# Performance work log

Hardware: AMD Instinct MI355X
Metric: run time of the kernel (lower is better)

## Reference

```python
import jax, jax.numpy as jnp
from jax import lax
import numpy as np

D_STATE = 16
DT_RANK = 16
D_INNER = 512
D_MODEL = 256


def _silu(x):
    return x * jax.nn.sigmoid(x)


def _ln(x, g, b):
    mu = jnp.mean(x, -1, keepdims=True)
    v = jnp.mean((x - mu) ** 2, -1, keepdims=True)
    return (x - mu) / jnp.sqrt(v + 1e-5) * g + b


def _mamba(x, Win, Wc, bc, Wx, Wdt, bdt, Alog, Dp, Wout):
    # x: [B, T, 256]; mamba_ssm defaults: expand=2, d_state=16, d_conv=4
    B, T, _ = x.shape
    xz = x @ Win.T                       # [B,T,1024]
    xc, z = jnp.split(xz, 2, axis=-1)    # each [B,T,512]
    # causal depthwise conv over time
    xt = jnp.transpose(xc, (0, 2, 1))    # [B,512,T]
    xt = lax.conv_general_dilated(xt, Wc[:, None, :], (1,), [(3, 0)],
                                  feature_group_count=D_INNER,
                                  dimension_numbers=('NCH', 'OIH', 'NCH'))
    xc = _silu(jnp.transpose(xt + bc[None, :, None], (0, 2, 1)))  # [B,T,512]
    dbl = xc @ Wx.T                      # [B,T,48]
    dt = jax.nn.softplus(dbl[..., :DT_RANK] @ Wdt.T + bdt)        # [B,T,512]
    Bm = dbl[..., DT_RANK:DT_RANK + D_STATE]                      # [B,T,16]
    Cm = dbl[..., DT_RANK + D_STATE:]                             # [B,T,16]
    A = -jnp.exp(Alog)                   # [512,16]
    dA = jnp.exp(dt[..., None] * A)                               # [B,T,512,16]
    dBu = dt[..., None] * Bm[:, :, None, :] * xc[..., None]       # [B,T,512,16]

    def step(h, inp):
        dA_t, dBu_t, C_t = inp
        h = dA_t * h + dBu_t
        return h, jnp.einsum('bdn,bn->bd', h, C_t)

    h0 = jnp.zeros((B, D_INNER, D_STATE), x.dtype)
    _, ys = lax.scan(step, h0, (jnp.moveaxis(dA, 1, 0),
                                jnp.moveaxis(dBu, 1, 0),
                                jnp.moveaxis(Cm, 1, 0)))
    y = jnp.moveaxis(ys, 0, 1) + xc * Dp
    y = y * _silu(z)
    return y @ Wout.T


def _forward(x1, x2, x3, x4, audio_feature,
             ln_g, ln_b, in_proj_w, conv_w, conv_b, xproj_w,
             dt_w, dt_b, A_log, D, out_proj_w, gate_w, gate_b):
    bt = x1.shape[0]
    gates = []
    for i in range(4):          # 4 independent 3-layer Mamba encoders
        a = audio_feature
        for l in range(3):      # Mamba_channel_temporal_block: a = ln(a); a = a + mamba(a)
            a = _ln(a, ln_g[i, l], ln_b[i, l])
            a = a + _mamba(a, in_proj_w[i, l], conv_w[i, l], conv_b[i, l],
                           xproj_w[i, l], dt_w[i, l], dt_b[i, l],
                           A_log[i, l], D[i, l], out_proj_w[i, l])
        gates.append(_silu(a @ gate_w[i].T + gate_b[i]))  # [B,5,256]
    g1 = gates[0].reshape(bt, 256, 1, 1)
    g2 = jnp.transpose(gates[1], (1, 0, 2)).reshape(bt, 256, 1, 1)
    g3 = jnp.transpose(gates[2], (1, 0, 2)).reshape(bt, 256, 1, 1)
    g4 = jnp.transpose(gates[3], (1, 0, 2)).reshape(bt, 256, 1, 1)
    o1 = x1 + g1 * x1   # gamma = 1
    o2 = x2 + g2 * x2
    o3 = x3 + g3 * x3
    o4 = x4 + g4 * x4
    audio_flat = audio_feature.reshape(-1, D_MODEL)[:, :, None]  # [bt,256,1]
    return (o4, o3, o2, o1, audio_flat)


def setup_inputs() -> dict:
    key = jax.random.key(0)
    ks = jax.random.split(key, 16)
    f32 = jnp.float32
    inp = {
        'x1': jax.random.normal(ks[0], (80, 256, 56, 56), f32),
        'x2': jax.random.normal(ks[1], (80, 256, 28, 28), f32),
        'x3': jax.random.normal(ks[2], (80, 256, 14, 14), f32),
        'x4': jax.random.normal(ks[3], (80, 256, 7, 7), f32),
        'audio_feature': jax.random.normal(ks[4], (16, 5, 256), f32),
        'ln_g': jnp.ones((4, 3, 256), f32),
        'ln_b': jnp.zeros((4, 3, 256), f32),
        'in_proj_w': jax.random.normal(ks[5], (4, 3, 2 * D_INNER, 256), f32) * 0.02,
        'conv_w': jax.random.normal(ks[6], (4, 3, D_INNER, 4), f32) * 0.1,
        'conv_b': jax.random.normal(ks[7], (4, 3, D_INNER), f32) * 0.02,
        'xproj_w': jax.random.normal(ks[8], (4, 3, DT_RANK + 2 * D_STATE, D_INNER), f32) * 0.02,
        'dt_w': jax.random.normal(ks[9], (4, 3, D_INNER, DT_RANK), f32) * 0.02,
        'dt_b': jax.random.normal(ks[10], (4, 3, D_INNER), f32) * 0.1 - 2.0,
        'A_log': jnp.log(jnp.tile(jnp.arange(1, D_STATE + 1, dtype=f32), (4, 3, D_INNER, 1))),
        'D': jnp.ones((4, 3, D_INNER), f32),
        'out_proj_w': jax.random.normal(ks[11], (4, 3, 256, D_INNER), f32) * 0.02,
        'gate_w': jax.random.normal(ks[12], (4, 256, 256), f32) * 0.05,
        'gate_b': jnp.zeros((4, 256), f32),
    }
    return inp


def reference(x1, x2, x3, x4, audio_feature,
              ln_g, ln_b, in_proj_w, conv_w, conv_b, xproj_w,
              dt_w, dt_b, A_log, D, out_proj_w, gate_w, gate_b):
    return _forward(x1, x2, x3, x4, audio_feature,
                    ln_g, ln_b, in_proj_w, conv_w, conv_b, xproj_w,
                    dt_w, dt_b, A_log, D, out_proj_w, gate_w, gate_b)
```

## Files before the change

### kernel.cpp

```cpp
#include <hip/hip_runtime.h>
#include <hip/hip_bf16.h>
#include <math.h>


#define NTOK 80
#define DM   256
#define DI   512

typedef float f32x4 __attribute__((ext_vector_type(4)));

__device__ __forceinline__ float silu_f(float v) {
    return v / (1.f + expf(-v));
}
__device__ __forceinline__ float dot4v(f32x4 a, f32x4 b) {
    return a.x*b.x + a.y*b.y + a.z*b.z + a.w*b.w;
}
__device__ __forceinline__ unsigned pack2bf(float lo, float hi) {
    unsigned ul = __float_as_uint(lo), uh = __float_as_uint(hi);
    unsigned bl = (ul + 0x7FFFu + ((ul >> 16) & 1u)) >> 16;
    unsigned bh = (uh + 0x7FFFu + ((uh >> 16) & 1u)) >> 16;
    return bl | (bh << 16);
}
__device__ __forceinline__ f32x4 unpk4(unsigned x, unsigned y) {
    f32x4 r;
    r.x = __uint_as_float(x << 16); r.y = __uint_as_float(x & 0xFFFF0000u);
    r.z = __uint_as_float(y << 16); r.w = __uint_as_float(y & 0xFFFF0000u);
    return r;
}

#define OFF_SG    0
#define OFF_WIN8  81920
#define OFF_WOUT8 1654784
#define OFF_GW8   2441216
#define OFF_WXT   2572288
#define OFF_DBLP  2867200
#define OFF_OUTP  2928640
#define OFF_BAR   3256320

__global__ __launch_bounds__(256) void k_tr(const float* __restrict__ Win,
                                            const float* __restrict__ Wout,
                                            const float* __restrict__ Wx,
                                            const float* __restrict__ gw,
                                            float* __restrict__ ws) {
    __shared__ __align__(16) float SH[8256];
    int b = blockIdx.x, tid = threadIdx.x;
    if (b == 0) {
        unsigned* barp = (unsigned*)(ws + OFF_BAR);
        #pragma unroll
        for (int j = 0; j < 4; ++j) barp[j * 256 + tid] = 0u;
    }

    if (b < 608) {
        const float* src; unsigned* dst; int rowStride, Ctot, c0, k0;
        if (b < 384) {
            int il = b / 32, rest = b % 32, cb = rest >> 1, kh = rest & 1;
            src = Win + (size_t)il * 1024 * 256; rowStride = 256; Ctot = 1024;
            c0 = cb * 64; k0 = kh * 128;
            dst = (unsigned*)(ws + OFF_WIN8) + (size_t)il * 32768 * 4;
        } else if (b < 576) {
            int t = b - 384; int il = t / 16, rest = t % 16, cb = rest >> 2, kq = rest & 3;
            src = Wout + (size_t)il * 256 * 512; rowStride = 512; Ctot = 256;
            c0 = cb * 64; k0 = kq * 128;
            dst = (unsigned*)(ws + OFF_WOUT8) + (size_t)il * 16384 * 4;
        } else {
            int t = b - 576; int i = t / 8, rest = t % 8, cb = rest >> 1, kh = rest & 1;
            src = gw + (size_t)i * 256 * 256; rowStride = 256; Ctot = 256;
            c0 = cb * 64; k0 = kh * 128;
            dst = (unsigned*)(ws + OFF_GW8) + (size_t)i * 8192 * 4;
        }
        for (int idx = tid; idx < 64 * 32; idx += 256) {
            int row = idx >> 5, kq4 = idx & 31;
            const float4 v = *(const float4*)(src + (size_t)(c0 + row) * rowStride
                                              + k0 + kq4 * 4);
            float* f = SH + row * 129 + kq4 * 4;
            f[0] = v.x; f[1] = v.y; f[2] = v.z; f[3] = v.w;
        }
        __syncthreads();
        uint4* d4 = (uint4*)dst;
        for (int idx = tid; idx < 1024; idx += 256) {
            int k8l = idx >> 6, c = idx & 63;
            const float* f = SH + c * 129 + k8l * 8;
            uint4 o;
            o.x = pack2bf(f[0], f[1]); o.y = pack2bf(f[2], f[3]);
            o.z = pack2bf(f[4], f[5]); o.w = pack2bf(f[6], f[7]);
            d4[((size_t)(k0 / 8 + k8l)) * Ctot + c0 + c] = o;
        }
    } else {
        int bb = b - 608; int mat = bb >> 3, tile = bb & 7;
        const float4* src = (const float4*)Wx + (size_t)mat * 6144;
        float4* dst = (float4*)(ws + OFF_WXT) + (size_t)mat * 6144;
        int R = 48, C4 = 128, tilesC = 4;
        int r0 = (tile / tilesC) << 5, cc0 = (tile % tilesC) << 5;
        float4* t4 = (float4*)SH;
        int tx = tid & 31, ty = tid >> 5;
        #pragma unroll
        for (int j = 0; j < 4; ++j) {
            int r = ty + j * 8;
            if (r0 + r < R) t4[r * 33 + tx] = src[(size_t)(r0 + r) * C4 + cc0 + tx];
        }
        __syncthreads();
        #pragma unroll
        for (int j = 0; j < 4; ++j) {
            int cc = ty + j * 8;
            if (r0 + tx < R) dst[(size_t)(cc0 + cc) * R + r0 + tx] = t4[tx * 33 + cc];
        }
    }
}

__device__ __forceinline__ void gbar(unsigned* slot) {
    __syncthreads();
    if (threadIdx.x == 0) {
        __hip_atomic_fetch_add(slot, 1u, __ATOMIC_RELEASE, __HIP_MEMORY_SCOPE_AGENT);
        while (__hip_atomic_load(slot, __ATOMIC_RELAXED, __HIP_MEMORY_SCOPE_AGENT) < 4u)
            __builtin_amdgcn_s_sleep(1);
        (void)__hip_atomic_load(slot, __ATOMIC_ACQUIRE, __HIP_MEMORY_SCOPE_AGENT);
    }
    __syncthreads();
}

__global__ __launch_bounds__(512) void k_chain4b(
    const float* __restrict__ audio,
    const float* __restrict__ ln_g, const float* __restrict__ ln_b,
    const float* __restrict__ Wc,   const float* __restrict__ bc,
    const float* __restrict__ Wdt,  const float* __restrict__ bdt,
    const float* __restrict__ Alog, const float* __restrict__ Dp,
    const float* __restrict__ gb,   float* __restrict__ ws)
{
    int gid = blockIdx.x & 63;
    int q   = blockIdx.x >> 6;
    int i = gid & 3, b = gid >> 2;
    int tid = threadIdx.x, lane = tid & 63, wave = tid >> 6;
    int dq = q * 128;

    float* s_g  = ws + OFF_SG;
    float* dblp = ws + OFF_DBLP + (size_t)gid * 4 * 240;
    float* outp = ws + OFF_OUTP + (size_t)gid * 4 * 1280;
    unsigned* bar = (unsigned*)(ws + OFF_BAR) + gid * 16;

    __shared__ __align__(16) float a_l   [1280];
    __shared__ __align__(16) float aln_l [1280];
    __shared__ __align__(16) float xz_l  [1280];
    __shared__ __align__(16) float xc_l  [640];
    __shared__ __align__(16) float y_l   [640];
    __shared__ __align__(16) float dbl_l [240];
    __shared__ __align__(16) float xp_l  [480];
    __shared__ __align__(16) float part_l[5120];

    if (tid < 320)
        ((f32x4*)a_l)[tid] = ((const f32x4*)(audio + (size_t)b * 1280))[tid];
    __syncthreads();

    for (int l = 0; l < 3; ++l) {
        int il = i * 3 + l;

        if (wave < 5) {
            f32x4 x = ((f32x4*)a_l)[wave*64 + lane];
            float s = x.x + x.y + x.z + x.w;
            #pragma unroll
            for (int o = 32; o > 0; o >>= 1) s += __shfl_down(s, o, 64);
            float mu = __shfl(s, 0, 64) * (1.f/256.f);
            f32x4 d = x - mu;
            float v2 = d.x*d.x + d.y*d.y + d.z*d.z + d.w*d.w;
            #pragma unroll
            for (int o = 32; o > 0; o >>= 1) v2 += __shfl_down(v2, o, 64);
            float rstd = rsqrtf(__shfl(v2, 0, 64) * (1.f/256.f) + 1e-5f);
            f32x4 g4 = ((const f32x4*)(ln_g + (size_t)il*DM))[lane];
            f32x4 b4 = ((const f32x4*)(ln_b + (size_t)il*DM))[lane];
            ((f32x4*)aln_l)[wave*64 + lane] = d * rstd * g4 + b4;
        }
        __syncthreads();

        {
            int cp = tid & 127, kq = tid >> 7;
            int lc, cA;
            if (cp < 64) { lc = 2*cp;       cA = dq + 2*cp; }
            else         { lc = 2*cp;       cA = 512 + dq + 2*(cp-64); }
            const uint4* W8 = (const uint4*)(ws + OFF_WIN8) + (size_t)il * 32768;
            const f32x4* a4 = (const f32x4*)aln_l;
            float accA[5] = {0,0,0,0,0}, accB[5] = {0,0,0,0,0};
            #pragma unroll
            for (int j = 0; j < 8; ++j) {
                int k8 = kq*8 + j;
                uint4 wa = W8[(size_t)k8*1024 + cA];
                uint4 wb = W8[(size_t)k8*1024 + cA + 1];
                f32x4 wa0 = unpk4(wa.x, wa.y), wa1 = unpk4(wa.z, wa.w);
                f32x4 wb0 = unpk4(wb.x, wb.y), wb1 = unpk4(wb.z, wb.w);
                #pragma unroll
                for (int r = 0; r < 5; ++r) {
                    f32x4 a0 = a4[r*64 + k8*2], a1 = a4[r*64 + k8*2 + 1];
                    accA[r] += dot4v(wa0, a0) + dot4v(wa1, a1);
                    accB[r] += dot4v(wb0, a0) + dot4v(wb1, a1);
                }
            }
            #pragma unroll
            for (int r = 0; r < 5; ++r) {
                part_l[kq*1280 + r*256 + lc]     = accA[r];
                part_l[kq*1280 + r*256 + lc + 1] = accB[r];
            }
        }
        __syncthreads();
        for (int v = tid; v < 1280; v += 512)
            xz_l[v] = part_l[v] + part_l[1280+v] + part_l[2560+v] + part_l[3840+v];
        __syncthreads();

        for (int v = tid; v < 640; v += 512) {
            int r = v >> 7, dl = v & 127;
            int ch = dq + dl;
            const float* wr = Wc + ((size_t)il*DI + ch)*4;
            float acc = bc[(size_t)il*DI + ch] + wr[3]*xz_l[r*256 + dl];
            if (r >= 1) acc += wr[2]*xz_l[(r-1)*256 + dl];
            if (r >= 2) acc += wr[1]*xz_l[(r-2)*256 + dl];
            if (r >= 3) acc += wr[0]*xz_l[(r-3)*256 + dl];
            xc_l[r*128 + dl] = silu_f(acc);
        }
        __syncthreads();

        if (tid < 480) {
            int c = tid % 48, r = (tid / 48) % 5, kh = tid / 240;
            const f32x4* wp = (const f32x4*)(ws + OFF_WXT) + (size_t)il*6144 + c;
            const f32x4* x4 = (const f32x4*)xc_l + r*32 + kh*16;
            float acc = 0.f;
            #pragma unroll
            for (int kk = 0; kk < 16; ++kk)
                acc += dot4v(wp[(size_t)(q*32 + kh*16 + kk)*48], x4[kk]);
            xp_l[tid] = acc;
        }
        __syncthreads();
        if (tid < 240) dblp[q*240 + tid] = xp_l[tid] + xp_l[240 + tid];
        gbar(bar + 2*l);
        if (tid < 240)
            dbl_l[tid] = dblp[tid] + dblp[240+tid] + dblp[480+tid] + dblp[720+tid];
        __syncthreads();

        if (tid < 128) {
            int d = dq + tid;
            float A[16], h[16];
            const f32x4* al4 = (const f32x4*)(Alog + ((size_t)il*DI + d)*16);
            f32x4 av0 = al4[0], av1 = al4[1], av2 = al4[2], av3 = al4[3];
            A[0]=-expf(av0.x); A[1]=-expf(av0.y); A[2]=-expf(av0.z); A[3]=-expf(av0.w);
            A[4]=-expf(av1.x); A[5]=-expf(av1.y); A[6]=-expf(av1.z); A[7]=-expf(av1.w);
            A[8]=-expf(av2.x); A[9]=-expf(av2.y); A[10]=-expf(av2.z); A[11]=-expf(av2.w);
            A[12]=-expf(av3.x); A[13]=-expf(av3.y); A[14]=-expf(av3.z); A[15]=-expf(av3.w);
            #pragma unroll
            for (int n = 0; n < 16; ++n) h[n] = 0.f;
            const f32x4* wd4 = (const f32x4*)(Wdt + ((size_t)il*DI + d)*16);
            f32x4 w0 = wd4[0], w1 = wd4[1], w2 = wd4[2], w3 = wd4[3];
            float bdtv = bdt[(size_t)il*DI + d];
            float dv   = Dp[(size_t)il*DI + d];
            #pragma unroll
            for (int t = 0; t < 5; ++t) {
                const float* db = dbl_l + t*48;
                float acc = bdtv;
                acc += db[0]*w0.x + db[1]*w0.y + db[2]*w0.z + db[3]*w0.w;
                acc += db[4]*w1.x + db[5]*w1.y + db[6]*w1.z + db[7]*w1.w;
                acc += db[8]*w2.x + db[9]*w2.y + db[10]*w2.z + db[11]*w2.w;
                acc += db[12]*w3.x + db[13]*w3.y + db[14]*w3.z + db[15]*w3.w;
                float dtv = fmaxf(acc, 0.f) + log1pf(expf(-fabsf(acc)));
                float xv  = xc_l[t*128 + tid];
                float zv  = xz_l[t*256 + 128 + tid];
                float dx  = dtv * xv;
                float yacc = 0.f;
                #pragma unroll
                for (int n = 0; n < 16; ++n) {
                    h[n] = expf(dtv*A[n])*h[n] + dx*db[16 + n];
                    yacc += h[n]*db[32 + n];
                }
                y_l[t*128 + tid] = (yacc + xv*dv) * silu_f(zv);
            }
        }
        __syncthreads();

        {
            int cp = tid & 127, kq = tid >> 7;
            int cA = 2*cp;
            const uint4* W8 = (const uint4*)(ws + OFF_WOUT8) + (size_t)il * 16384;
            const f32x4* y4 = (const f32x4*)y_l;
            float accA[5] = {0,0,0,0,0}, accB[5] = {0,0,0,0,0};
            #pragma unroll
            for (int j = 0; j < 4; ++j) {
                int k8l = kq*4 + j;
                int k8g = q*16 + k8l;
                uint4 wa = W8[(size_t)k8g*256 + cA];
                uint4 wb = W8[(size_t)k8g*256 + cA + 1];
                f32x4 wa0 = unpk4(wa.x, wa.y), wa1 = unpk4(wa.z, wa.w);
                f32x4 wb0 = unpk4(wb.x, wb.y), wb1 = unpk4(wb.z, wb.w);
                #pragma unroll
                for (int r = 0; r < 5; ++r) {
                    f32x4 y0 = y4[r*32 + k8l*2], y1 = y4[r*32 + k8l*2 + 1];
                    accA[r] += dot4v(wa0, y0) + dot4v(wa1, y1);
                    accB[r] += dot4v(wb0, y0) + dot4v(wb1, y1);
                }
            }
            #pragma unroll
            for (int r = 0; r < 5; ++r) {
                part_l[kq*1280 + r*256 + cA]     = accA[r];
                part_l[kq*1280 + r*256 + cA + 1] = accB[r];
            }
        }
        __syncthreads();
        for (int v = tid; v < 1280; v += 512)
            outp[q*1280 + v] = part_l[v] + part_l[1280+v] + part_l[2560+v] + part_l[3840+v];
        gbar(bar + 2*l + 1);
        for (int v = tid; v < 1280; v += 512)
            a_l[v] = aln_l[v] + outp[v] + outp[1280+v] + outp[2560+v] + outp[3840+v];
        __syncthreads();
    }

    {
        int cp = tid & 31, kq = tid >> 5;
        int gA = q*64 + 2*cp;
        const uint4* G8 = (const uint4*)(ws + OFF_GW8) + (size_t)i * 8192;
        const f32x4* a4 = (const f32x4*)a_l;
        float accA[5] = {0,0,0,0,0}, accB[5] = {0,0,0,0,0};
        #pragma unroll
        for (int j = 0; j < 2; ++j) {
            int k8 = kq*2 + j;
            uint4 wa = G8[(size_t)k8*256 + gA];
            uint4 wb = G8[(size_t)k8*256 + gA + 1];
            f32x4 wa0 = unpk4(wa.x, wa.y), wa1 = unpk4(wa.z, wa.w);
            f32x4 wb0 = unpk4(wb.x, wb.y), wb1 = unpk4(wb.z, wb.w);
            #pragma unroll
            for (int r = 0; r < 5; ++r) {
                f32x4 a0 = a4[r*64 + k8*2], a1 = a4[r*64 + k8*2 + 1];
                accA[r] += dot4v(wa0, a0) + dot4v(wa1, a1);
                accB[r] += dot4v(wb0, a0) + dot4v(wb1, a1);
            }
        }
        #pragma unroll
        for (int r = 0; r < 5; ++r) {
            part_l[kq*320 + r*64 + 2*cp]     = accA[r];
            part_l[kq*320 + r*64 + 2*cp + 1] = accB[r];
        }
    }
    __syncthreads();
    if (tid < 320) {
        int r = tid >> 6, lc = tid & 63;
        float s = gb[(size_t)i*DM + q*64 + lc];
        #pragma unroll
        for (int kq = 0; kq < 16; ++kq) s += part_l[kq*320 + tid];
        int row = b*5 + r;
        int np  = (i == 0) ? row : (r*16 + b);
        s_g[((size_t)i*NTOK + np)*DM + q*64 + lc] = 1.f + silu_f(s);
    }
}

__global__ __launch_bounds__(256) void k_elem(
    const float* __restrict__ x1, const float* __restrict__ x2,
    const float* __restrict__ x3, const float* __restrict__ x4,
    const float* __restrict__ audio, const float* __restrict__ s_g,
    float* __restrict__ out) {
    int b = blockIdx.x;
    int t = threadIdx.x;

    if (b < 512) {
        const float* s = s_g + 3 * NTOK * DM;
        const f32x4* xv = (const f32x4*)x4;
        f32x4* ov = (f32x4*)out;
        const int total4 = 1003520 / 4;
        for (int v = b * 256 + t; v < total4; v += 512 * 256) {
            f32x4 x = __builtin_nontemporal_load(&xv[v]);
#pragma unroll
            for (int j = 0; j < 4; ++j) {
                int idx = v * 4 + j;
                x[j] *= s[idx / 49];
            }
            __builtin_nontemporal_store(x, &ov[v]);
        }
    } else if (b < 1024) {
        const float* s = s_g + 2 * NTOK * DM;
        const f32x4* xv = (const f32x4*)x3;
        f32x4* ov = (f32x4*)(out + 1003520);
        const int total4 = 4014080 / 4;
        for (int v = (b - 512) * 256 + t; v < total4; v += 512 * 256) {
            float f = s[v / 49];
            f32x4 x = __builtin_nontemporal_load(&xv[v]);
            x *= f;
            __builtin_nontemporal_store(x, &ov[v]);
        }
    } else if (b < 2048) {
        const float* s = s_g + 1 * NTOK * DM;
        const f32x4* xv = (const f32x4*)x2;
        f32x4* ov = (f32x4*)(out + 5017600);
        const int total4 = 16056320 / 4;
        for (int v = (b - 1024) * 256 + t; v < total4; v += 1024 * 256) {
            float f = s[v / 196];
            f32x4 x = __builtin_nontemporal_load(&xv[v]);
            x *= f;
            __builtin_nontemporal_store(x, &ov[v]);
        }
    } else if (b < 6144) {
        const float* s = s_g;
        const f32x4* xv = (const f32x4*)x1;
        f32x4* ov = (f32x4*)(out + 21073920);
        const int total4 = 64225280 / 4;
        for (int v = (b - 2048) * 256 + t; v < total4; v += 4096 * 256) {
            float f = s[v / 784];
            f32x4 x = __builtin_nontemporal_load(&xv[v]);
            x *= f;
            __builtin_nontemporal_store(x, &ov[v]);
        }
    } else {
        int idx = (b - 6144) * 256 + t;
        out[85299200 + idx] = audio[idx];
    }
}

extern "C" void kernel_launch(void* const* d_in, const int* in_sizes, int n_in,
                              void* d_out, int out_size, void* d_ws, size_t ws_size,
                              hipStream_t stream) {
    const float* x1        = (const float*)d_in[0];
    const float* x2        = (const float*)d_in[1];
    const float* x3        = (const float*)d_in[2];
    const float* x4        = (const float*)d_in[3];
    const float* audio     = (const float*)d_in[4];
    const float* ln_g      = (const float*)d_in[5];
    const float* ln_b      = (const float*)d_in[6];
    const float* in_proj_w = (const float*)d_in[7];
    const float* conv_w    = (const float*)d_in[8];
    const float* conv_b    = (const float*)d_in[9];
    const float* xproj_w   = (const float*)d_in[10];
    const float* dt_w      = (const float*)d_in[11];
    const float* dt_b      = (const float*)d_in[12];
    const float* A_log     = (const float*)d_in[13];
    const float* Dvec      = (const float*)d_in[14];
    const float* out_proj_w= (const float*)d_in[15];
    const float* gate_w    = (const float*)d_in[16];
    const float* gate_b    = (const float*)d_in[17];

    float* ws = (float*)d_ws;

    k_tr<<<704, 256, 0, stream>>>(in_proj_w, out_proj_w, xproj_w, gate_w, ws);
    k_chain4b<<<256, 512, 0, stream>>>(audio, ln_g, ln_b, conv_w, conv_b,
                                       dt_w, dt_b, A_log, Dvec, gate_b, ws);
    k_elem<<<6224, 256, 0, stream>>>(x1, x2, x3, x4, audio, ws + OFF_SG,
                                     (float*)d_out);
}
```

Baseline: 238.9 us.

## Merge four cooperating blocks per chain into one 1024-thread block, drop global barriers

Each (batch, encoder) chain previously ran on four 512-thread blocks that exchanged partial results through global memory with atomic spin barriers twice per layer. Now one 1024-thread block handles the full 512-channel width, so the barriers, global partial buffers and barrier reset go away. The GEMV inner loops are also restructured to 4 columns per lane with a cross-lane shuffle reduction instead of shared-memory partial sums. The cost is only 64 blocks on the GPU, so less parallelism for the weight streaming and the selective scan. Each thread also carries more serial work.

After: 554.0 us. +131.9%, slower.

```diff
diff --git a/kernel.cpp b/kernel.cpp
--- a/kernel.cpp
+++ b/kernel.cpp
@@ -33,9 +33,6 @@
 #define OFF_WOUT8 1654784
 #define OFF_GW8   2441216
 #define OFF_WXT   2572288
-#define OFF_DBLP  2867200
-#define OFF_OUTP  2928640
-#define OFF_BAR   3256320
 
 __global__ __launch_bounds__(256) void k_tr(const float* __restrict__ Win,
                                             const float* __restrict__ Wout,
@@ -44,11 +41,6 @@
                                             float* __restrict__ ws) {
     __shared__ __align__(16) float SH[8256];
     int b = blockIdx.x, tid = threadIdx.x;
-    if (b == 0) {
-        unsigned* barp = (unsigned*)(ws + OFF_BAR);
-        #pragma unroll
-        for (int j = 0; j < 4; ++j) barp[j * 256 + tid] = 0u;
-    }
 
     if (b < 608) {
         const float* src; unsigned* dst; int rowStride, Ctot, c0, k0;
@@ -107,18 +99,7 @@
     }
 }
 
-__device__ __forceinline__ void gbar(unsigned* slot) {
-    __syncthreads();
-    if (threadIdx.x == 0) {
-        __hip_atomic_fetch_add(slot, 1u, __ATOMIC_RELEASE, __HIP_MEMORY_SCOPE_AGENT);
-        while (__hip_atomic_load(slot, __ATOMIC_RELAXED, __HIP_MEMORY_SCOPE_AGENT) < 4u)
-            __builtin_amdgcn_s_sleep(1);
-        (void)__hip_atomic_load(slot, __ATOMIC_ACQUIRE, __HIP_MEMORY_SCOPE_AGENT);
-    }
-    __syncthreads();
-}
-
-__global__ __launch_bounds__(512) void k_chain4b(
+__global__ __launch_bounds__(1024, 4) void k_chain1k(
     const float* __restrict__ audio,
     const float* __restrict__ ln_g, const float* __restrict__ ln_b,
     const float* __restrict__ Wc,   const float* __restrict__ bc,
@@ -126,25 +107,19 @@
     const float* __restrict__ Alog, const float* __restrict__ Dp,
     const float* __restrict__ gb,   float* __restrict__ ws)
 {
-    int gid = blockIdx.x & 63;
-    int q   = blockIdx.x >> 6;
-    int i = gid & 3, b = gid >> 2;
-    int tid = threadIdx.x, lane = tid & 63, wave = tid >> 6;
-    int dq = q * 128;
-
-    float* s_g  = ws + OFF_SG;
-    float* dblp = ws + OFF_DBLP + (size_t)gid * 4 * 240;
-    float* outp = ws + OFF_OUTP + (size_t)gid * 4 * 1280;
-    unsigned* bar = (unsigned*)(ws + OFF_BAR) + gid * 16;
-
-    __shared__ __align__(16) float a_l   [1280];
-    __shared__ __align__(16) float aln_l [1280];
-    __shared__ __align__(16) float xz_l  [1280];
-    __shared__ __align__(16) float xc_l  [640];
-    __shared__ __align__(16) float y_l   [640];
-    __shared__ __align__(16) float dbl_l [240];
-    __shared__ __align__(16) float xp_l  [480];
-    __shared__ __align__(16) float part_l[5120];
+    int blk = blockIdx.x;
+    int i = blk & 3, b = blk >> 2;
+    int tid = threadIdx.x, lane = tid & 63, wv = tid >> 6;
+
+    float* s_g = ws + OFF_SG;
+
+    __shared__ __align__(16) float a_l  [1280];
+    __shared__ __align__(16) float aln_l[1280];
+    __shared__ __align__(16) float xz_l [5120];
+    __shared__ __align__(16) float xc_l [2560];
+    __shared__ __align__(16) float y_l  [2560];
+    __shared__ __align__(16) float dbl_l[240];
+    __shared__ __align__(16) float xp_l [960];
 
     if (tid < 320)
         ((f32x4*)a_l)[tid] = ((const f32x4*)(audio + (size_t)b * 1280))[tid];
@@ -153,8 +128,8 @@
     for (int l = 0; l < 3; ++l) {
         int il = i * 3 + l;
 
-        if (wave < 5) {
-            f32x4 x = ((f32x4*)a_l)[wave*64 + lane];
+        if (wv < 5) {
+            f32x4 x = ((f32x4*)a_l)[wv*64 + lane];
             float s = x.x + x.y + x.z + x.w;
             #pragma unroll
             for (int o = 32; o > 0; o >>= 1) s += __shfl_down(s, o, 64);
@@ -166,74 +141,84 @@
             float rstd = rsqrtf(__shfl(v2, 0, 64) * (1.f/256.f) + 1e-5f);
             f32x4 g4 = ((const f32x4*)(ln_g + (size_t)il*DM))[lane];
             f32x4 b4 = ((const f32x4*)(ln_b + (size_t)il*DM))[lane];
-            ((f32x4*)aln_l)[wave*64 + lane] = d * rstd * g4 + b4;
+            ((f32x4*)aln_l)[wv*64 + lane] = d * rstd * g4 + b4;
         }
         __syncthreads();
 
         {
-            int cp = tid & 127, kq = tid >> 7;
-            int lc, cA;
-            if (cp < 64) { lc = 2*cp;       cA = dq + 2*cp; }
-            else         { lc = 2*cp;       cA = 512 + dq + 2*(cp-64); }
+            int cq = lane & 15, kq = lane >> 4;
+            int col0 = wv * 64 + cq * 4;
             const uint4* W8 = (const uint4*)(ws + OFF_WIN8) + (size_t)il * 32768;
             const f32x4* a4 = (const f32x4*)aln_l;
-            float accA[5] = {0,0,0,0,0}, accB[5] = {0,0,0,0,0};
-            #pragma unroll
-            for (int j = 0; j < 8; ++j) {
-                int k8 = kq*8 + j;
-                uint4 wa = W8[(size_t)k8*1024 + cA];
-                uint4 wb = W8[(size_t)k8*1024 + cA + 1];
-                f32x4 wa0 = unpk4(wa.x, wa.y), wa1 = unpk4(wa.z, wa.w);
-                f32x4 wb0 = unpk4(wb.x, wb.y), wb1 = unpk4(wb.z, wb.w);
+            float acc[5][4];
+            #pragma unroll
+            for (int r = 0; r < 5; ++r)
+                #pragma unroll
+                for (int j = 0; j < 4; ++j) acc[r][j] = 0.f;
+            #pragma unroll
+            for (int t8 = 0; t8 < 8; ++t8) {
+                int k8 = kq * 8 + t8;
+                f32x4 wl[4], wh[4];
+                #pragma unroll
+                for (int j = 0; j < 4; ++j) {
+                    uint4 w = W8[(size_t)k8 * 1024 + col0 + j];
+                    wl[j] = unpk4(w.x, w.y); wh[j] = unpk4(w.z, w.w);
+                }
                 #pragma unroll
                 for (int r = 0; r < 5; ++r) {
-                    f32x4 a0 = a4[r*64 + k8*2], a1 = a4[r*64 + k8*2 + 1];
-                    accA[r] += dot4v(wa0, a0) + dot4v(wa1, a1);
-                    accB[r] += dot4v(wb0, a0) + dot4v(wb1, a1);
-                }
-            }
-            #pragma unroll
-            for (int r = 0; r < 5; ++r) {
-                part_l[kq*1280 + r*256 + lc]     = accA[r];
-                part_l[kq*1280 + r*256 + lc + 1] = accB[r];
-            }
-        }
-        __syncthreads();
-        for (int v = tid; v < 1280; v += 512)
-            xz_l[v] = part_l[v] + part_l[1280+v] + part_l[2560+v] + part_l[3840+v];
-        __syncthreads();
-
-        for (int v = tid; v < 640; v += 512) {
-            int r = v >> 7, dl = v & 127;
-            int ch = dq + dl;
-            const float* wr = Wc + ((size_t)il*DI + ch)*4;
-            float acc = bc[(size_t)il*DI + ch] + wr[3]*xz_l[r*256 + dl];
-            if (r >= 1) acc += wr[2]*xz_l[(r-1)*256 + dl];
-            if (r >= 2) acc += wr[1]*xz_l[(r-2)*256 + dl];
-            if (r >= 3) acc += wr[0]*xz_l[(r-3)*256 + dl];
-            xc_l[r*128 + dl] = silu_f(acc);
-        }
-        __syncthreads();
-
-        if (tid < 480) {
+                    f32x4 x0 = a4[r*64 + k8*2], x1 = a4[r*64 + k8*2 + 1];
+                    #pragma unroll
+                    for (int j = 0; j < 4; ++j)
+                        acc[r][j] += dot4v(wl[j], x0) + dot4v(wh[j], x1);
+                }
+            }
+            #pragma unroll
+            for (int r = 0; r < 5; ++r)
+                #pragma unroll
+                for (int j = 0; j < 4; ++j) {
+                    float v = acc[r][j];
+                    v += __shfl_xor(v, 16, 64);
+                    v += __shfl_xor(v, 32, 64);
+                    acc[r][j] = v;
+                }
+            if (kq == 0) {
+                #pragma unroll
+                for (int r = 0; r < 5; ++r) {
+                    f32x4 o = {acc[r][0], acc[r][1], acc[r][2], acc[r][3]};
+                    ((f32x4*)xz_l)[r*256 + (col0 >> 2)] = o;
+                }
+            }
+        }
+        __syncthreads();
+
+        for (int v = tid; v < 2560; v += 1024) {
+            int r = v >> 9, dl = v & 511;
+            const float* wr = Wc + ((size_t)il*DI + dl)*4;
+            float acc = bc[(size_t)il*DI + dl] + wr[3]*xz_l[r*1024 + dl];
+            if (r >= 1) acc += wr[2]*xz_l[(r-1)*1024 + dl];
+            if (r >= 2) acc += wr[1]*xz_l[(r-2)*1024 + dl];
+            if (r >= 3) acc += wr[0]*xz_l[(r-3)*1024 + dl];
+            xc_l[r*512 + dl] = silu_f(acc);
+        }
+        __syncthreads();
+
+        if (tid < 960) {
             int c = tid % 48, r = (tid / 48) % 5, kh = tid / 240;
             const f32x4* wp = (const f32x4*)(ws + OFF_WXT) + (size_t)il*6144 + c;
-            const f32x4* x4 = (const f32x4*)xc_l + r*32 + kh*16;
+            const f32x4* x4 = (const f32x4*)xc_l + r*128 + kh*32;
             float acc = 0.f;
             #pragma unroll
-            for (int kk = 0; kk < 16; ++kk)
-                acc += dot4v(wp[(size_t)(q*32 + kh*16 + kk)*48], x4[kk]);
+            for (int kk = 0; kk < 32; ++kk)
+                acc += dot4v(wp[(size_t)(kh*32 + kk)*48], x4[kk]);
             xp_l[tid] = acc;
         }
         __syncthreads();
-        if (tid < 240) dblp[q*240 + tid] = xp_l[tid] + xp_l[240 + tid];
-        gbar(bar + 2*l);
         if (tid < 240)
-            dbl_l[tid] = dblp[tid] + dblp[240+tid] + dblp[480+tid] + dblp[720+tid];
-        __syncthreads();
-
-        if (tid < 128) {
-            int d = dq + tid;
+            dbl_l[tid] = xp_l[tid] + xp_l[240+tid] + xp_l[480+tid] + xp_l[720+tid];
+        __syncthreads();
+
+        if (tid < 512) {
+            int d = tid;
             float A[16], h[16];
             const f32x4* al4 = (const f32x4*)(Alog + ((size_t)il*DI + d)*16);
             f32x4 av0 = al4[0], av1 = al4[1], av2 = al4[2], av3 = al4[3];
@@ -256,8 +241,8 @@
                 acc += db[8]*w2.x + db[9]*w2.y + db[10]*w2.z + db[11]*w2.w;
                 acc += db[12]*w3.x + db[13]*w3.y + db[14]*w3.z + db[15]*w3.w;
                 float dtv = fmaxf(acc, 0.f) + log1pf(expf(-fabsf(acc)));
-                float xv  = xc_l[t*128 + tid];
-                float zv  = xz_l[t*256 + 128 + tid];
+                float xv  = xc_l[t*512 + d];
+                float zv  = xz_l[t*1024 + 512 + d];
                 float dx  = dtv * xv;
                 float yacc = 0.f;
                 #pragma unroll
@@ -265,82 +250,119 @@
                     h[n] = expf(dtv*A[n])*h[n] + dx*db[16 + n];
                     yacc += h[n]*db[32 + n];
                 }
-                y_l[t*128 + tid] = (yacc + xv*dv) * silu_f(zv);
+                y_l[t*512 + d] = (yacc + xv*dv) * silu_f(zv);
             }
         }
         __syncthreads();
 
         {
-            int cp = tid & 127, kq = tid >> 7;
-            int cA = 2*cp;
+            int cq = lane & 15, kqi = lane >> 4;
+            int qg = (wv & 3) * 16 + cq;
+            int kg = wv >> 2;
+            int kq = kg * 4 + kqi;
+            int col0 = qg * 4;
             const uint4* W8 = (const uint4*)(ws + OFF_WOUT8) + (size_t)il * 16384;
             const f32x4* y4 = (const f32x4*)y_l;
-            float accA[5] = {0,0,0,0,0}, accB[5] = {0,0,0,0,0};
-            #pragma unroll
-            for (int j = 0; j < 4; ++j) {
-                int k8l = kq*4 + j;
-                int k8g = q*16 + k8l;
-                uint4 wa = W8[(size_t)k8g*256 + cA];
-                uint4 wb = W8[(size_t)k8g*256 + cA + 1];
-                f32x4 wa0 = unpk4(wa.x, wa.y), wa1 = unpk4(wa.z, wa.w);
-                f32x4 wb0 = unpk4(wb.x, wb.y), wb1 = unpk4(wb.z, wb.w);
+            float acc[5][4];
+            #pragma unroll
+            for (int r = 0; r < 5; ++r)
+                #pragma unroll
+                for (int j = 0; j < 4; ++j) acc[r][j] = 0.f;
+            #pragma unroll
+            for (int t8 = 0; t8 < 4; ++t8) {
+                int k8 = kq * 4 + t8;
+                f32x4 wl[4], wh[4];
+                #pragma unroll
+                for (int j = 0; j < 4; ++j) {
+                    uint4 w = W8[(size_t)k8 * 256 + col0 + j];
+                    wl[j] = unpk4(w.x, w.y); wh[j] = unpk4(w.z, w.w);
+                }
                 #pragma unroll
                 for (int r = 0; r < 5; ++r) {
-                    f32x4 y0 = y4[r*32 + k8l*2], y1 = y4[r*32 + k8l*2 + 1];
-                    accA[r] += dot4v(wa0, y0) + dot4v(wa1, y1);
-                    accB[r] += dot4v(wb0, y0) + dot4v(wb1, y1);
-                }
-            }
-            #pragma unroll
-            for (int r = 0; r < 5; ++r) {
-                part_l[kq*1280 + r*256 + cA]     = accA[r];
-                part_l[kq*1280 + r*256 + cA + 1] = accB[r];
-            }
-        }
-        __syncthreads();
-        for (int v = tid; v < 1280; v += 512)
-            outp[q*1280 + v] = part_l[v] + part_l[1280+v] + part_l[2560+v] + part_l[3840+v];
-        gbar(bar + 2*l + 1);
-        for (int v = tid; v < 1280; v += 512)
-            a_l[v] = aln_l[v] + outp[v] + outp[1280+v] + outp[2560+v] + outp[3840+v];
+                    f32x4 x0 = y4[r*128 + k8*2], x1 = y4[r*128 + k8*2 + 1];
+                    #pragma unroll
+                    for (int j = 0; j < 4; ++j)
+                        acc[r][j] += dot4v(wl[j], x0) + dot4v(wh[j], x1);
+                }
+            }
+            #pragma unroll
+            for (int r = 0; r < 5; ++r)
+                #pragma unroll
+                for (int j = 0; j < 4; ++j) {
+                    float v = acc[r][j];
+                    v += __shfl_xor(v, 16, 64);
+                    v += __shfl_xor(v, 32, 64);
+                    acc[r][j] = v;
+                }
+            if (kqi == 0) {
+                #pragma unroll
+                for (int r = 0; r < 5; ++r) {
+                    f32x4 o = {acc[r][0], acc[r][1], acc[r][2], acc[r][3]};
+                    ((f32x4*)xz_l)[kg*320 + r*64 + qg] = o;
+                }
+            }
+        }
+        __syncthreads();
+        for (int v = tid; v < 1280; v += 1024)
+            a_l[v] = aln_l[v] + xz_l[v] + xz_l[1280+v] + xz_l[2560+v] + xz_l[3840+v];
         __syncthreads();
     }
 
     {
-        int cp = tid & 31, kq = tid >> 5;
-        int gA = q*64 + 2*cp;
+        int cq = lane & 15, kqi = lane >> 4;
+        int qg = (wv & 3) * 16 + cq;
+        int kg = wv >> 2;
+        int kq = kg * 4 + kqi;
+        int col0 = qg * 4;
         const uint4* G8 = (const uint4*)(ws + OFF_GW8) + (size_t)i * 8192;
         const f32x4* a4 = (const f32x4*)a_l;
-        float accA[5] = {0,0,0,0,0}, accB[5] = {0,0,0,0,0};
+        float acc[5][4];
         #pragma unroll
-        for (int j = 0; j < 2; ++j) {
-            int k8 = kq*2 + j;
-            uint4 wa = G8[(size_t)k8*256 + gA];
-            uint4 wb = G8[(size_t)k8*256 + gA + 1];
-            f32x4 wa0 = unpk4(wa.x, wa.y), wa1 = unpk4(wa.z, wa.w);
-            f32x4 wb0 = unpk4(wb.x, wb.y), wb1 = unpk4(wb.z, wb.w);
+        for (int r = 0; r < 5; ++r)
+            #pragma unroll
+            for (int j = 0; j < 4; ++j) acc[r][j] = 0.f;
+        #pragma unroll
+        for (int t8 = 0; t8 < 2; ++t8) {
+            int k8 = kq * 2 + t8;
+            f32x4 wl[4], wh[4];
+            #pragma unroll
+            for (int j = 0; j < 4; ++j) {
+                uint4 w = G8[(size_t)k8 * 256 + col0 + j];
+                wl[j] = unpk4(w.x, w.y); wh[j] = unpk4(w.z, w.w);
+            }
             #pragma unroll
             for (int r = 0; r < 5; ++r) {
-                f32x4 a0 = a4[r*64 + k8*2], a1 = a4[r*64 + k8*2 + 1];
-                accA[r] += dot4v(wa0, a0) + dot4v(wa1, a1);
-                accB[r] += dot4v(wb0, a0) + dot4v(wb1, a1);
+                f32x4 x0 = a4[r*64 + k8*2], x1 = a4[r*64 + k8*2 + 1];
+                #pragma unroll
+                for (int j = 0; j < 4; ++j)
+                    acc[r][j] += dot4v(wl[j], x0) + dot4v(wh[j], x1);
             }
         }
         #pragma unroll
-        for (int r = 0; r < 5; ++r) {
-            part_l[kq*320 + r*64 + 2*cp]     = accA[r];
-            part_l[kq*320 + r*64 + 2*cp + 1] = accB[r];
+        for (int r = 0; r < 5; ++r)
+            #pragma unroll
+            for (int j = 0; j < 4; ++j) {
+                float v = acc[r][j];
+                v += __shfl_xor(v, 16, 64);
+                v += __shfl_xor(v, 32, 64);
+                acc[r][j] = v;
+            }
+        if (kqi == 0) {
+            #pragma unroll
+            for (int r = 0; r < 5; ++r) {
+                f32x4 o = {acc[r][0], acc[r][1], acc[r][2], acc[r][3]};
+                ((f32x4*)xz_l)[kg*320 + r*64 + qg] = o;
+            }
         }
     }
     __syncthreads();
-    if (tid < 320) {
-        int r = tid >> 6, lc = tid & 63;
-        float s = gb[(size_t)i*DM + q*64 + lc];
-        #pragma unroll
-        for (int kq = 0; kq < 16; ++kq) s += part_l[kq*320 + tid];
+    for (int v = tid; v < 1280; v += 1024) {
+        int r = v >> 8, c = v & 255;
+        float val = gb[(size_t)i*DM + c]
+                  + xz_l[v] + xz_l[1280+v] + xz_l[2560+v] + xz_l[3840+v];
         int row = b*5 + r;
         int np  = (i == 0) ? row : (r*16 + b);
-        s_g[((size_t)i*NTOK + np)*DM + q*64 + lc] = 1.f + silu_f(s);
+        s_g[((size_t)i*NTOK + np)*DM + c] = 1.f + silu_f(val);
     }
 }
 
@@ -430,7 +452,7 @@
     float* ws = (float*)d_ws;
 
     k_tr<<<704, 256, 0, stream>>>(in_proj_w, out_proj_w, xproj_w, gate_w, ws);
-    k_chain4b<<<256, 512, 0, stream>>>(audio, ln_g, ln_b, conv_w, conv_b,
+    k_chain1k<<<64, 1024, 0, stream>>>(audio, ln_g, ln_b, conv_w, conv_b,
                                        dt_w, dt_b, A_log, Dvec, gate_b, ws);
     k_elem<<<6224, 256, 0, stream>>>(x1, x2, x3, x4, audio, ws + OFF_SG,
                                      (float*)d_out);
```
